# Kernel tuning notes

Measured on AMD Instinct MI355X. Metric: run time of the kernel, lower is better.

## Reference

```python
import jax, jax.numpy as jnp
import numpy as np

NINP, NHID, NTOK, NLAYERS, BSZ = 4096, 512, 50257, 2, 32
T_ENC, T_DEC = 80, 40


def lstm_layer(x, h0, c0, Wih, Whh, b):
    """Single LSTM layer over a [T,B,in] sequence; PyTorch gate order i,f,g,o."""
    def step(carry, xt):
        h, c = carry
        z = xt @ Wih.T + h @ Whh.T + b  # [B, 4H]
        i, f, g, o = jnp.split(z, 4, axis=-1)
        c = jax.nn.sigmoid(f) * c + jax.nn.sigmoid(i) * jnp.tanh(g)
        h = jax.nn.sigmoid(o) * jnp.tanh(c)
        return (h, c), h
    (hN, cN), ys = jax.lax.scan(step, (h0, c0), x)
    return ys, hN, cN


def multi_lstm(x, h0, c0, params):
    """Stacked LSTM; params = list of (Wih, Whh, b) per layer."""
    hs, cs = [], []
    y = x
    for l, (Wih, Whh, b) in enumerate(params):
        y, hN, cN = lstm_layer(y, h0[l], c0[l], Wih, Whh, b)
        hs.append(hN); cs.append(cN)
    return y, jnp.stack(hs), jnp.stack(cs)


def setup_inputs():
    key = jax.random.key(0)
    ks = iter(jax.random.split(key, 32))
    def rn(shape, scale=0.05):
        return (jax.random.normal(next(ks), shape, dtype=jnp.float32) * scale)
    H4 = 4 * NHID
    d = {}
    d["inp"] = rn((T_ENC, BSZ, NINP), 1.0)
    for name in ("hid1_h", "hid1_c", "hid2_h", "hid2_c"):
        d[name] = jnp.zeros((NLAYERS, BSZ, NHID), jnp.float32)
    # lstm1: layer0 in=NINP, layer1 in=NHID (b = b_ih + b_hh fused)
    d["l1_Wih0"] = rn((H4, NINP)); d["l1_Whh0"] = rn((H4, NHID)); d["l1_b0"] = rn((H4,))
    d["l1_Wih1"] = rn((H4, NHID)); d["l1_Whh1"] = rn((H4, NHID)); d["l1_b1"] = rn((H4,))
    # lstm2: layer0 in=2*NHID, layer1 in=NHID
    d["l2_Wih0"] = rn((H4, 2 * NHID)); d["l2_Whh0"] = rn((H4, NHID)); d["l2_b0"] = rn((H4,))
    d["l2_Wih1"] = rn((H4, NHID)); d["l2_Whh1"] = rn((H4, NHID)); d["l2_b1"] = rn((H4,))
    d["W_out"] = rn((NTOK, NHID)); d["b_out"] = rn((NTOK,))
    d["W_emb"] = rn((NHID, NTOK)); d["b_emb"] = rn((NHID,))
    d["target_len"] = T_DEC
    return d


def reference(inp, hid1_h, hid1_c, hid2_h, hid2_c,
              l1_Wih0, l1_Whh0, l1_b0, l1_Wih1, l1_Whh1, l1_b1,
              l2_Wih0, l2_Whh0, l2_b0, l2_Wih1, l2_Whh1, l2_b1,
              W_out, b_out, W_emb, b_emb, target_len):
    p1 = [(l1_Wih0, l1_Whh0, l1_b0), (l1_Wih1, l1_Whh1, l1_b1)]
    p2 = [(l2_Wih0, l2_Whh0, l2_b0), (l2_Wih1, l2_Whh1, l2_b1)]
    T, B, ninp = inp.shape
    H = hid1_h.shape[-1]
    # --- encoding stage ---
    out1, h1, c1 = multi_lstm(inp, hid1_h, hid1_c, p1)
    pad_h = jnp.zeros((T, B, H), inp.dtype)
    _, h2, c2 = multi_lstm(jnp.concatenate([pad_h, out1], axis=-1), hid2_h, hid2_c, p2)
    # --- decoding stage ---
    pad_in = jnp.zeros((target_len, B, ninp), inp.dtype)
    out1d, _, _ = multi_lstm(pad_in, h1, c1, p1)
    # vocab2emb(one-hot BOS at index 0) = W_emb[:, 0] + b_emb; never updated in
    # the original loop (variable-name bug), so it is constant over decode steps,
    # making the per-step loop equivalent to one lstm2 scan.
    bos_emb = W_emb[:, 0] + b_emb  # [H]
    bos = jnp.broadcast_to(bos_emb, (target_len, B, H))
    out2d, _, _ = multi_lstm(jnp.concatenate([bos, out1d], axis=-1), h2, c2, p2)
    logits = jnp.einsum('tbh,vh->tbv', out2d, W_out) + b_out  # [T_dec, B, V]
    return jax.nn.log_softmax(logits, axis=-1)
```

## Files before the change

kernel.cpp:

```cpp
#include <hip/hip_runtime.h>
#include <hip/hip_bf16.h>
#include <cstddef>

#define NINP 4096
#define NHID 512
#define G4   2048
#define NTOK 50257
#define BSZ  32
#define T_ENC 80
#define T_DEC 40

typedef __attribute__((ext_vector_type(4))) float  f32x4;
typedef __attribute__((ext_vector_type(4))) __bf16 bf16x4;
typedef __attribute__((ext_vector_type(8))) __bf16 bf16x8;

__device__ __forceinline__ int sw_off(int r, int k) {
    return r * 128 + ((((k >> 3) ^ (r & 7)) << 4) | ((k & 7) << 1));
}
__device__ __forceinline__ int swA(int r, int k) {
    return r * 256 + ((((k >> 3) ^ (r & 7)) << 4) | ((k & 7) << 1));
}
__device__ __forceinline__ int sw512(int r, int k) {
    return r * 1024 + ((((k >> 3) ^ (r & 7)) << 4) | ((k & 7) << 1));
}

__device__ __forceinline__ void split4(const float4& v, bf16x4& h, bf16x4& l) {
    float a0 = v.x, a1 = v.y, a2 = v.z, a3 = v.w;
    __bf16 h0 = (__bf16)a0, h1 = (__bf16)a1, h2 = (__bf16)a2, h3 = (__bf16)a3;
    h[0] = h0; h[1] = h1; h[2] = h2; h[3] = h3;
    l[0] = (__bf16)(a0 - (float)h0);
    l[1] = (__bf16)(a1 - (float)h1);
    l[2] = (__bf16)(a2 - (float)h2);
    l[3] = (__bf16)(a3 - (float)h3);
}

__device__ __forceinline__ bf16x4 hi4(const float4& v) {
    bf16x4 h; h[0] = (__bf16)v.x; h[1] = (__bf16)v.y;
    h[2] = (__bf16)v.z; h[3] = (__bf16)v.w; return h;
}

__device__ __forceinline__ void split8(const float4& a, const float4& b,
                                       bf16x8& h, bf16x8& l) {
    float x[8] = {a.x, a.y, a.z, a.w, b.x, b.y, b.z, b.w};
    #pragma unroll
    for (int i = 0; i < 8; i++) {
        __bf16 hb = (__bf16)x[i];
        h[i] = hb; l[i] = (__bf16)(x[i] - (float)hb);
    }
}

__device__ __forceinline__ bf16x8 to_bf16x8(const float4& a, const float4& b) {
    bf16x8 r;
    r[0]=(__bf16)a.x; r[1]=(__bf16)a.y; r[2]=(__bf16)a.z; r[3]=(__bf16)a.w;
    r[4]=(__bf16)b.x; r[5]=(__bf16)b.y; r[6]=(__bf16)b.z; r[7]=(__bf16)b.w;
    return r;
}

__device__ __forceinline__ void unpack8(const uint4& a, const uint4& b,
                                        bf16x8& h, bf16x8& l) {
    unsigned u[8] = {a.x, a.y, a.z, a.w, b.x, b.y, b.z, b.w};
    union { unsigned short s; __bf16 v; } t;
    #pragma unroll
    for (int i = 0; i < 8; i++) {
        t.s = (unsigned short)(u[i] & 0xffff); h[i] = t.v;
        t.s = (unsigned short)(u[i] >> 16);    l[i] = t.v;
    }
}
__device__ __forceinline__ bf16x8 unpack_hi8(const uint4& a, const uint4& b) {
    unsigned u[8] = {a.x, a.y, a.z, a.w, b.x, b.y, b.z, b.w};
    union { unsigned short s; __bf16 v; } t;
    bf16x8 h;
    #pragma unroll
    for (int i = 0; i < 8; i++) { t.s = (unsigned short)(u[i] & 0xffff); h[i] = t.v; }
    return h;
}

__device__ __forceinline__ unsigned pack_hilo(float x) {
    __bf16 hb = (__bf16)x;
    float hf = (float)hb;
    __bf16 lb = (__bf16)(x - hf);
    union { __bf16 b; unsigned short s; } ch, cl;
    ch.b = hb; cl.b = lb;
    return (unsigned)ch.s | ((unsigned)cl.s << 16);
}

__device__ __forceinline__ float fast_sigmoid(float x) {
    return 1.f / (1.f + __expf(-x));
}
__device__ __forceinline__ float fast_tanh(float x) {
    return 1.f - 2.f / (__expf(2.f * x) + 1.f);
}

__global__ __launch_bounds__(256) void gemm_hilo(
    const float* __restrict__ A, int lda,
    const float* __restrict__ B, int ldb,
    const float* __restrict__ bias,
    float* __restrict__ Z, int ldz,
    int N, int K)
{
    __shared__ __align__(16) char lds[49152];
    const int tid  = threadIdx.x;
    const int bm   = blockIdx.y * 128;
    const int bn   = blockIdx.x * 128;
    const int wave = tid >> 6;
    const int lane = tid & 63;
    const int wm   = (wave >> 1) * 64;
    const int wn   = (wave & 1) * 64;
    const int lr   = lane & 15;
    const int kg   = lane >> 4;

    const int rr = tid >> 4;
    const int kk = (tid & 15) * 4;

    f32x4 acc[4][4] = {};

    for (int k0 = 0; k0 < K; k0 += 64) {
        float4 av[8], bv[8];
        #pragma unroll
        for (int i = 0; i < 8; i++) {
            int r = i * 16 + rr;
            av[i] = *(const float4*)&A[(size_t)(bm + r) * lda + k0 + kk];
            int rb = bn + r;
            if (rb < N)
                bv[i] = *(const float4*)&B[(size_t)rb * ldb + k0 + kk];
            else
                bv[i] = make_float4(0.f, 0.f, 0.f, 0.f);
        }
        __syncthreads();
        #pragma unroll
        for (int i = 0; i < 8; i++) {
            int r = i * 16 + rr;
            int off = sw_off(r, kk);
            bf16x4 h, l;
            split4(av[i], h, l);
            *(bf16x4*)(lds + off)         = h;
            *(bf16x4*)(lds + 16384 + off) = l;
            *(bf16x4*)(lds + 32768 + off) = hi4(bv[i]);
        }
        __syncthreads();
        #pragma unroll
        for (int ks = 0; ks < 2; ks++) {
            bf16x8 ah[4], al[4], bh[4];
            const int kbase = ks * 32 + kg * 8;
            #pragma unroll
            for (int f = 0; f < 4; f++) {
                int offA = sw_off(wm + f * 16 + lr, kbase);
                ah[f] = *(const bf16x8*)(lds + offA);
                al[f] = *(const bf16x8*)(lds + 16384 + offA);
                int offB = sw_off(wn + f * 16 + lr, kbase);
                bh[f] = *(const bf16x8*)(lds + 32768 + offB);
            }
            #pragma unroll
            for (int fm = 0; fm < 4; fm++)
                #pragma unroll
                for (int fn = 0; fn < 4; fn++) {
                    acc[fm][fn] = __builtin_amdgcn_mfma_f32_16x16x32_bf16(
                        ah[fm], bh[fn], acc[fm][fn], 0, 0, 0);
                    acc[fm][fn] = __builtin_amdgcn_mfma_f32_16x16x32_bf16(
                        al[fm], bh[fn], acc[fm][fn], 0, 0, 0);
                }
        }
    }

    #pragma unroll
    for (int fn = 0; fn < 4; fn++) {
        int col = bn + wn + fn * 16 + lr;
        if (col < N) {
            float bb = bias ? bias[col] : 0.f;
            #pragma unroll
            for (int fm = 0; fm < 4; fm++) {
                #pragma unroll
                for (int j = 0; j < 4; j++) {
                    int row = bm + wm + fm * 16 + kg * 4 + j;
                    Z[(size_t)row * ldz + col] = acc[fm][fn][j] + bb;
                }
            }
        }
    }
}

__global__ __launch_bounds__(256, 1) void gemm_vocab(
    const __bf16* __restrict__ Ah,
    const float* __restrict__ B,
    const float* __restrict__ bias,
    float* __restrict__ Z)
{
    __shared__ __align__(16) char lds[163840];
    char* ldsB = lds;
    char* ldsA = lds + 131072;

    const int tid  = threadIdx.x;
    const int bn   = blockIdx.x * 128;
    const int wave = tid >> 6;
    const int lane = tid & 63;
    const int wm   = (wave >> 1) * 64;
    const int wn   = (wave & 1) * 64;
    const int lr   = lane & 15;
    const int kg   = lane >> 4;

    #pragma unroll 4
    for (int jj = 0; jj < 32; jj++) {
        int e = tid + jj * 256;
        int row = e >> 6;
        int k = (e & 63) * 8;
        int gr = bn + row;
        float4 v0, v1;
        if (gr < NTOK) {
            v0 = *(const float4*)&B[(size_t)gr * 512 + k];
            v1 = *(const float4*)&B[(size_t)gr * 512 + k + 4];
        } else {
            v0 = make_float4(0.f,0.f,0.f,0.f); v1 = v0;
        }
        *(bf16x8*)(ldsB + sw512(row, k)) = to_bf16x8(v0, v1);
    }

    float bb[4];
    #pragma unroll
    for (int fn = 0; fn < 4; fn++) {
        int col = bn + wn + fn * 16 + lr;
        bb[fn] = (col < NTOK) ? bias[col] : 0.f;
    }
    __syncthreads();

    for (int mt = 0; mt < 10; mt++) {
        f32x4 acc[4][4] = {};
        for (int k0 = 0; k0 < 4; k0++) {
            __syncthreads();
            #pragma unroll
            for (int jj = 0; jj < 8; jj++) {
                int e = tid + jj * 256;
                int row = e >> 4;
                int k = (e & 15) * 8;
                uint4 v = *(const uint4*)&Ah[(size_t)(mt * 128 + row) * 512 + k0 * 128 + k];
                *(uint4*)(ldsA + swA(row, k)) = v;
            }
            __syncthreads();
            #pragma unroll
            for (int ks = 0; ks < 4; ks++) {
                bf16x8 ah[4], bh[4];
                const int ka = ks * 32 + kg * 8;
                #pragma unroll
                for (int f = 0; f < 4; f++) {
                    ah[f] = *(const bf16x8*)(ldsA + swA(wm + f * 16 + lr, ka));
                    bh[f] = *(const bf16x8*)(ldsB + sw512(wn + f * 16 + lr, k0 * 128 + ka));
                }
                #pragma unroll
                for (int fm = 0; fm < 4; fm++)
                    #pragma unroll
                    for (int fn = 0; fn < 4; fn++)
                        acc[fm][fn] = __builtin_amdgcn_mfma_f32_16x16x32_bf16(
                            ah[fm], bh[fn], acc[fm][fn], 0, 0, 0);
            }
        }
        #pragma unroll
        for (int fn = 0; fn < 4; fn++) {
            int col = bn + wn + fn * 16 + lr;
            if (col < NTOK) {
                #pragma unroll
                for (int fm = 0; fm < 4; fm++) {
                    #pragma unroll
                    for (int j = 0; j < 4; j++) {
                        int row = mt * 128 + wm + fm * 16 + kg * 4 + j;
                        Z[(size_t)row * NTOK + col] = acc[fm][fn][j] + bb[fn];
                    }
                }
            }
        }
    }
}

__device__ __forceinline__ void grid_barrier(unsigned* flags, unsigned* gen,
                                             unsigned target)
{
    __syncthreads();
    if (threadIdx.x == 0) {
        __builtin_amdgcn_fence(__ATOMIC_RELEASE, "agent");
        __hip_atomic_store(&flags[blockIdx.x], target, __ATOMIC_RELAXED,
                           __HIP_MEMORY_SCOPE_AGENT);
    }
    if (blockIdx.x == 0) {
        while (__hip_atomic_load(&flags[threadIdx.x], __ATOMIC_RELAXED,
                                 __HIP_MEMORY_SCOPE_AGENT) < target)
            __builtin_amdgcn_s_sleep(1);
        __syncthreads();
        if (threadIdx.x == 0)
            __hip_atomic_store(gen, target, __ATOMIC_RELAXED,
                               __HIP_MEMORY_SCOPE_AGENT);
    }
    if (threadIdx.x == 0) {
        while (__hip_atomic_load(gen, __ATOMIC_RELAXED,
                                 __HIP_MEMORY_SCOPE_AGENT) < target)
            __builtin_amdgcn_s_sleep(1);
        __builtin_amdgcn_fence(__ATOMIC_ACQUIRE, "agent");
    }
    __syncthreads();
}

__global__ __launch_bounds__(256, 1) void fused_scan(
    const float* __restrict__ Zx,
    const float* __restrict__ Whh_0, const float* __restrict__ bias_0,
    const float* __restrict__ Wih_1, const float* __restrict__ Whh_1,
    const float* __restrict__ bias_1,
    const float* __restrict__ Wih_2, const float* __restrict__ Whh_2,
    const float* __restrict__ bias_2e, const float* __restrict__ bias_2d,
    const float* __restrict__ Wih_3, const float* __restrict__ Whh_3,
    const float* __restrict__ bias_3,
    const float* __restrict__ hid1_h, const float* __restrict__ hid1_c,
    const float* __restrict__ hid2_h, const float* __restrict__ hid2_c,
    __bf16* __restrict__ dec3h,
    unsigned* hbuf, unsigned* flags, unsigned* gen)
{
    __shared__ __align__(16) char lds[131072];
    float* a_x = (float*)(lds + 32768);

    const int tid  = threadIdx.x;
    const int L    = blockIdx.x >> 6;
    const int bidc = blockIdx.x & 63;
    const int wave = tid >> 6;
    const int lane = tid & 63;
    const int mh   = wave >> 1;
    const int nh   = wave & 1;
    const int lr   = lane & 15;
    const int kg   = lane >> 4;
    const int jcbase = bidc * 8;
    const int bq = tid >> 3;
    const int aq = tid & 7;

    const float* Whh = (L==0)?Whh_0:(L==1)?Whh_1:(L==2)?Whh_2:Whh_3;
    const float* Wih = (L==1)?Wih_1:(L==2)?Wih_2:(L==3)?Wih_3:nullptr;
    const int ld_ih  = (L==2)?1024:512;
    const float* be  = (L==0)?bias_0:(L==1)?bias_1:(L==2)?bias_2e:bias_3;
    const float* bd  = (L==2)?bias_2d:be;
    const float* h0  = ((L<2)?hid1_h:hid2_h) + (L&1)*16384;
    const float* c0  = ((L<2)?hid1_c:hid2_c) + (L&1)*16384;
    unsigned* myb       = hbuf + L*32768;
    const unsigned* xsb = hbuf + (L>0 ? (L-1)*32768 : 0);

    {
        int gate = (bq<8)?0:(bq<16)?2:(bq<24)?1:3;
        int row  = gate*512 + jcbase + (bq&7);
        const float* wr = Whh + (size_t)row * 512;
        #pragma unroll
        for (int jj = 0; jj < 8; jj++) {
            int k = aq*8 + jj*64;
            *(bf16x8*)(lds + 65536 + sw512(bq, k)) =
                to_bf16x8(*(const float4*)(wr+k), *(const float4*)(wr+k+4));
        }
        if (Wih) {
            const float* wr2 = Wih + (size_t)row * ld_ih;
            #pragma unroll
            for (int jj = 0; jj < 8; jj++) {
                int k = aq*8 + jj*64;
                *(bf16x8*)(lds + 98304 + sw512(bq, k)) =
                    to_bf16x8(*(const float4*)(wr2+k), *(const float4*)(wr2+k+4));
            }
        }
    }

    const int n_col = nh*16 + lr;
    const int gate  = (n_col<8)?0:(n_col<16)?2:(n_col<24)?1:3;
    const int col2048 = gate*512 + jcbase + (n_col & 7);
    const float bbe = be[col2048];
    const float bbd = bd[col2048];

    float cc[4] = {0.f, 0.f, 0.f, 0.f};
    if (nh == 1 && lr < 8) {
        #pragma unroll
        for (int j = 0; j < 4; j++)
            cc[j] = c0[(mh*16 + kg*4 + j)*512 + jcbase + lr];
    }
    __syncthreads();

    const int rowA = mh*16 + lr;
    const int rowB = nh*16 + lr;

    for (int tt = 0; tt < 123; ++tt) {
        const int myt = tt - L;
        if (myt >= 0 && myt < 120) {
            uint4 xr[8][2];
            if (L > 0) {
                const unsigned* xs = xsb + (size_t)(myt & 1)*16384 + bq*512;
                #pragma unroll
                for (int jj = 0; jj < 8; jj++) {
                    int k = aq*8 + jj*64;
                    xr[jj][0] = *(const uint4*)(xs + k);
                    xr[jj][1] = *(const uint4*)(xs + k + 4);
                }
            }
            if (myt == 0) {
                const float* hr = h0 + bq*512;
                #pragma unroll
                for (int jj = 0; jj < 8; jj++) {
                    int k = aq*8 + jj*64;
                    bf16x8 H, Lo;
                    split8(*(const float4*)(hr+k), *(const float4*)(hr+k+4), H, Lo);
                    int off = sw512(bq, k);
                    *(bf16x8*)(lds + off)         = H;
                    *(bf16x8*)(lds + 32768 + off) = Lo;
                }
            } else {
                const unsigned* hs = myb + (size_t)((myt-1) & 1)*16384 + bq*512;
                #pragma unroll
                for (int jj = 0; jj < 8; jj++) {
                    int k = aq*8 + jj*64;
                    bf16x8 H, Lo;
                    unpack8(*(const uint4*)(hs+k), *(const uint4*)(hs+k+4), H, Lo);
                    int off = sw512(bq, k);
                    *(bf16x8*)(lds + off)         = H;
                    *(bf16x8*)(lds + 32768 + off) = Lo;
                }
            }
            __syncthreads();

            f32x4 accA = {0.f,0.f,0.f,0.f}, accB = {0.f,0.f,0.f,0.f};
            #pragma unroll
            for (int ks = 0; ks < 16; ++ks) {
                int k = ks*32 + kg*8;
                int offA = sw512(rowA, k);
                int offB = sw512(rowB, k);
                bf16x8 ah = *(const bf16x8*)(lds + offA);
                bf16x8 al = *(const bf16x8*)(lds + 32768 + offA);
                bf16x8 bh = *(const bf16x8*)(lds + 65536 + offB);
                accA = __builtin_amdgcn_mfma_f32_16x16x32_bf16(ah, bh, accA, 0,0,0);
                accB = __builtin_amdgcn_mfma_f32_16x16x32_bf16(al, bh, accB, 0,0,0);
            }
            __syncthreads();

            if (L > 0) {
                #pragma unroll
                for (int jj = 0; jj < 8; jj++) {
                    int k = aq*8 + jj*64;
                    *(bf16x8*)(lds + sw512(bq, k)) = unpack_hi8(xr[jj][0], xr[jj][1]);
                }
                __syncthreads();
                #pragma unroll
                for (int ks = 0; ks < 16; ++ks) {
                    int k = ks*32 + kg*8;
                    bf16x8 ax = *(const bf16x8*)(lds + sw512(rowA, k));
                    bf16x8 bi = *(const bf16x8*)(lds + 98304 + sw512(rowB, k));
                    accA = __builtin_amdgcn_mfma_f32_16x16x32_bf16(ax, bi, accA, 0,0,0);
                }
            }

            const float bbv = (L == 2 && myt >= 80) ? bbd : bbe;
            float z[4];
            #pragma unroll
            for (int j = 0; j < 4; j++) {
                int b = mh*16 + kg*4 + j;
                float zx = (L == 0 && myt < 80)
                    ? Zx[(size_t)myt*(BSZ*G4) + b*G4 + col2048] : 0.f;
                z[j] = accA[j] + accB[j] + bbv + zx;
            }

            if (nh == 0) {
                float zo[4];
                #pragma unroll
                for (int j = 0; j < 4; j++) zo[j] = __shfl_xor(z[j], 8);
                if (lr < 8) {
                    #pragma unroll
                    for (int j = 0; j < 4; j++)
                        a_x[(mh*16 + kg*4 + j)*8 + lr] =
                            fast_sigmoid(z[j]) * fast_tanh(zo[j]);
                }
            }
            __syncthreads();

            if (nh == 1) {
                float cnew[4] = {0.f,0.f,0.f,0.f};
                if (lr < 8) {
                    #pragma unroll
                    for (int j = 0; j < 4; j++) {
                        float av = a_x[(mh*16 + kg*4 + j)*8 + lr];
                        cnew[j] = fast_sigmoid(z[j]) * cc[j] + av;
                        cc[j] = cnew[j];
                    }
                }
                float cfrom[4];
                #pragma unroll
                for (int j = 0; j < 4; j++) cfrom[j] = __shfl_xor(cnew[j], 8);
                if (lr >= 8) {
                    #pragma unroll
                    for (int j = 0; j < 4; j++) {
                        float hn = fast_sigmoid(z[j]) * fast_tanh(cfrom[j]);
                        int b = mh*16 + kg*4 + j;
                        int hcol = jcbase + (lr - 8);
                        if (L == 3 && myt >= 80)
                            dec3h[(size_t)(myt-80)*(BSZ*NHID) + b*512 + hcol] =
                                (__bf16)hn;
                        __hip_atomic_store(&myb[(size_t)(myt & 1)*16384 + b*512 + hcol],
                                           pack_hilo(hn), __ATOMIC_RELAXED,
                                           __HIP_MEMORY_SCOPE_AGENT);
                    }
                }
            }
        }
        grid_barrier(flags, gen, (unsigned)tt + 1u);
    }
}

__global__ __launch_bounds__(256) void bias2_kernel(
    const float* __restrict__ W_emb,
    const float* __restrict__ b_emb,
    const float* __restrict__ Wih0,
    const float* __restrict__ b0,
    float* __restrict__ bias2)
{
    __shared__ float bos[NHID];
    const int tid = threadIdx.x;
    for (int i = tid; i < NHID; i += 256)
        bos[i] = W_emb[(size_t)i * NTOK] + b_emb[i];
    __syncthreads();
    int j = blockIdx.x * 256 + tid;
    float acc = b0[j];
    for (int k = 0; k < NHID; k++)
        acc += bos[k] * Wih0[(size_t)j * 1024 + k];
    bias2[j] = acc;
}

__global__ __launch_bounds__(256) void logsoftmax_kernel(float* __restrict__ logits)
{
    const size_t row = blockIdx.x;
    float* p = logits + row * (size_t)NTOK;
    const int tid = threadIdx.x;

    float m = -1e30f, s = 0.f;
    for (int i = tid; i < NTOK; i += 256) {
        float x = p[i];
        float mn = fmaxf(m, x);
        s = s * __expf(m - mn) + __expf(x - mn);
        m = mn;
    }
    #pragma unroll
    for (int off = 32; off > 0; off >>= 1) {
        float mo = __shfl_down(m, off);
        float so = __shfl_down(s, off);
        float mn = fmaxf(m, mo);
        s = s * __expf(m - mn) + so * __expf(mo - mn);
        m = mn;
    }
    __shared__ float sm[4], ss[4];
    if ((tid & 63) == 0) { sm[tid >> 6] = m; ss[tid >> 6] = s; }
    __syncthreads();
    float M4 = fmaxf(fmaxf(sm[0], sm[1]), fmaxf(sm[2], sm[3]));
    float S  = ss[0] * __expf(sm[0] - M4) + ss[1] * __expf(sm[1] - M4)
             + ss[2] * __expf(sm[2] - M4) + ss[3] * __expf(sm[3] - M4);
    float lse = M4 + logf(S);
    for (int i = tid; i < NTOK; i += 256) p[i] = p[i] - lse;
}

extern "C" void kernel_launch(void* const* d_in, const int* in_sizes, int n_in,
                              void* d_out, int out_size, void* d_ws, size_t ws_size,
                              hipStream_t stream)
{
    const float* inp     = (const float*)d_in[0];
    const float* hid1_h  = (const float*)d_in[1];
    const float* hid1_c  = (const float*)d_in[2];
    const float* hid2_h  = (const float*)d_in[3];
    const float* hid2_c  = (const float*)d_in[4];
    const float* l1_Wih0 = (const float*)d_in[5];
    const float* l1_Whh0 = (const float*)d_in[6];
    const float* l1_b0   = (const float*)d_in[7];
    const float* l1_Wih1 = (const float*)d_in[8];
    const float* l1_Whh1 = (const float*)d_in[9];
    const float* l1_b1   = (const float*)d_in[10];
    const float* l2_Wih0 = (const float*)d_in[11];
    const float* l2_Whh0 = (const float*)d_in[12];
    const float* l2_b0   = (const float*)d_in[13];
    const float* l2_Wih1 = (const float*)d_in[14];
    const float* l2_Whh1 = (const float*)d_in[15];
    const float* l2_b1   = (const float*)d_in[16];
    const float* W_out   = (const float*)d_in[17];
    const float* b_out   = (const float*)d_in[18];
    const float* W_emb   = (const float*)d_in[19];
    const float* b_emb   = (const float*)d_in[20];

    float* out = (float*)d_out;
    float* ws  = (float*)d_ws;

    float* Zx    = ws;
    float* bias2 = ws + 5242880;
    __bf16* dec3h = (__bf16*)(ws + 5244928);
    unsigned* hbuf  = (unsigned*)(ws + 5572608);
    unsigned* flags = (unsigned*)(ws + 5703680);
    unsigned* gen   = flags + 256;

    (void)hipMemsetAsync(flags, 0, 1028, stream);

    {
        dim3 grid((G4 + 127) / 128, (T_ENC * BSZ) / 128);
        gemm_hilo<<<grid, dim3(256), 0, stream>>>(
            inp, NINP, l1_Wih0, NINP, nullptr, Zx, G4, G4, NINP);
    }
    bias2_kernel<<<8, 256, 0, stream>>>(W_emb, b_emb, l2_Wih0, l2_b0, bias2);

    fused_scan<<<256, 256, 0, stream>>>(
        Zx,
        l1_Whh0, l1_b0,
        l1_Wih1, l1_Whh1, l1_b1,
        l2_Wih0 + 512, l2_Whh0, l2_b0, bias2,
        l2_Wih1, l2_Whh1, l2_b1,
        hid1_h, hid1_c, hid2_h, hid2_c,
        dec3h, hbuf, flags, gen);

    gemm_vocab<<<(NTOK + 127) / 128, dim3(256), 0, stream>>>(
        dec3h, W_out, b_out, out);
    logsoftmax_kernel<<<1280, dim3(256), 0, stream>>>(out);
}
```

Before: 1.956 ms.

## Drop A low-part split in input GEMM, prefetch Zx, spin barrier without sleep

The input-projection GEMM no longer splits A into bf16 hi+lo parts. This halves the MFMA count and cuts LDS use, at the cost of accuracy in the projection (A is now plain bf16). It also adds a trailing __syncthreads that the loop needed to be race-free. The fused scan prefetches the next step's Zx values into registers so the global load leaves the critical path, and the block-0 barrier poll drops s_sleep to lower barrier latency.

```diff
diff --git a/kernel.cpp b/kernel.cpp
--- a/kernel.cpp
+++ b/kernel.cpp
@@ -22,16 +22,6 @@
 }
 __device__ __forceinline__ int sw512(int r, int k) {
     return r * 1024 + ((((k >> 3) ^ (r & 7)) << 4) | ((k & 7) << 1));
-}
-
-__device__ __forceinline__ void split4(const float4& v, bf16x4& h, bf16x4& l) {
-    float a0 = v.x, a1 = v.y, a2 = v.z, a3 = v.w;
-    __bf16 h0 = (__bf16)a0, h1 = (__bf16)a1, h2 = (__bf16)a2, h3 = (__bf16)a3;
-    h[0] = h0; h[1] = h1; h[2] = h2; h[3] = h3;
-    l[0] = (__bf16)(a0 - (float)h0);
-    l[1] = (__bf16)(a1 - (float)h1);
-    l[2] = (__bf16)(a2 - (float)h2);
-    l[3] = (__bf16)(a3 - (float)h3);
 }
 
 __device__ __forceinline__ bf16x4 hi4(const float4& v) {
@@ -91,14 +81,14 @@
     return 1.f - 2.f / (__expf(2.f * x) + 1.f);
 }
 
-__global__ __launch_bounds__(256) void gemm_hilo(
+__global__ __launch_bounds__(256) void gemm_ahi(
     const float* __restrict__ A, int lda,
     const float* __restrict__ B, int ldb,
     const float* __restrict__ bias,
     float* __restrict__ Z, int ldz,
     int N, int K)
 {
-    __shared__ __align__(16) char lds[49152];
+    __shared__ __align__(16) char lds[32768];
     const int tid  = threadIdx.x;
     const int bm   = blockIdx.y * 128;
     const int bn   = blockIdx.x * 128;
@@ -131,35 +121,27 @@
         for (int i = 0; i < 8; i++) {
             int r = i * 16 + rr;
             int off = sw_off(r, kk);
-            bf16x4 h, l;
-            split4(av[i], h, l);
-            *(bf16x4*)(lds + off)         = h;
-            *(bf16x4*)(lds + 16384 + off) = l;
-            *(bf16x4*)(lds + 32768 + off) = hi4(bv[i]);
+            *(bf16x4*)(lds + off)         = hi4(av[i]);
+            *(bf16x4*)(lds + 16384 + off) = hi4(bv[i]);
         }
         __syncthreads();
         #pragma unroll
         for (int ks = 0; ks < 2; ks++) {
-            bf16x8 ah[4], al[4], bh[4];
+            bf16x8 ah[4], bh[4];
             const int kbase = ks * 32 + kg * 8;
             #pragma unroll
             for (int f = 0; f < 4; f++) {
-                int offA = sw_off(wm + f * 16 + lr, kbase);
-                ah[f] = *(const bf16x8*)(lds + offA);
-                al[f] = *(const bf16x8*)(lds + 16384 + offA);
-                int offB = sw_off(wn + f * 16 + lr, kbase);
-                bh[f] = *(const bf16x8*)(lds + 32768 + offB);
+                ah[f] = *(const bf16x8*)(lds + sw_off(wm + f * 16 + lr, kbase));
+                bh[f] = *(const bf16x8*)(lds + 16384 + sw_off(wn + f * 16 + lr, kbase));
             }
             #pragma unroll
             for (int fm = 0; fm < 4; fm++)
                 #pragma unroll
-                for (int fn = 0; fn < 4; fn++) {
+                for (int fn = 0; fn < 4; fn++)
                     acc[fm][fn] = __builtin_amdgcn_mfma_f32_16x16x32_bf16(
                         ah[fm], bh[fn], acc[fm][fn], 0, 0, 0);
-                    acc[fm][fn] = __builtin_amdgcn_mfma_f32_16x16x32_bf16(
-                        al[fm], bh[fn], acc[fm][fn], 0, 0, 0);
-                }
-        }
+        }
+        __syncthreads();
     }
 
     #pragma unroll
@@ -281,7 +263,7 @@
     if (blockIdx.x == 0) {
         while (__hip_atomic_load(&flags[threadIdx.x], __ATOMIC_RELAXED,
                                  __HIP_MEMORY_SCOPE_AGENT) < target)
-            __builtin_amdgcn_s_sleep(1);
+            ;
         __syncthreads();
         if (threadIdx.x == 0)
             __hip_atomic_store(gen, target, __ATOMIC_RELAXED,
@@ -369,6 +351,13 @@
         for (int j = 0; j < 4; j++)
             cc[j] = c0[(mh*16 + kg*4 + j)*512 + jcbase + lr];
     }
+
+    float zxr[4] = {0.f, 0.f, 0.f, 0.f};
+    if (L == 0) {
+        #pragma unroll
+        for (int j = 0; j < 4; j++)
+            zxr[j] = Zx[(size_t)(mh*16 + kg*4 + j)*G4 + col2048];
+    }
     __syncthreads();
 
     const int rowA = mh*16 + lr;
@@ -445,11 +434,18 @@
             const float bbv = (L == 2 && myt >= 80) ? bbd : bbe;
             float z[4];
             #pragma unroll
-            for (int j = 0; j < 4; j++) {
-                int b = mh*16 + kg*4 + j;
-                float zx = (L == 0 && myt < 80)
-                    ? Zx[(size_t)myt*(BSZ*G4) + b*G4 + col2048] : 0.f;
-                z[j] = accA[j] + accB[j] + bbv + zx;
+            for (int j = 0; j < 4; j++)
+                z[j] = accA[j] + accB[j] + bbv
+                     + ((L == 0 && myt < 80) ? zxr[j] : 0.f);
+
+            {
+                int mytn = myt + 1;
+                if (L == 0 && mytn < 80) {
+                    #pragma unroll
+                    for (int j = 0; j < 4; j++)
+                        zxr[j] = Zx[(size_t)mytn*(BSZ*G4)
+                                    + (mh*16+kg*4+j)*G4 + col2048];
+                }
             }
 
             if (nh == 0) {
@@ -588,7 +584,7 @@
 
     {
         dim3 grid((G4 + 127) / 128, (T_ENC * BSZ) / 128);
-        gemm_hilo<<<grid, dim3(256), 0, stream>>>(
+        gemm_ahi<<<grid, dim3(256), 0, stream>>>(
             inp, NINP, l1_Wih0, NINP, nullptr, Zx, G4, G4, NINP);
     }
     bias2_kernel<<<8, 256, 0, stream>>>(W_emb, b_emb, l2_Wih0, l2_b0, bias2);
```

New measurement: 1.914 ms. 2.1% less time.
